# Performance work log

Hardware: AMD Instinct MI355X
Metric: run time of the kernel (lower is better)

## Reference

```python
import jax, jax.numpy as jnp
import numpy as np

B, T, C, H, L, V = 8, 512, 512, 8, 2, 512
DH = C // H
SCALE = 1.0 / np.sqrt(DH)


def _ln(x, g, b):
    mu = jnp.mean(x, -1, keepdims=True)
    var = jnp.mean((x - mu) ** 2, -1, keepdims=True)
    return (x - mu) * jax.lax.rsqrt(var + 1e-5) * g + b


def setup_inputs() -> dict:
    key = jax.random.key(0)
    ks = jax.random.split(key, 16)
    f = lambda k, shape: jax.random.normal(k, shape, jnp.float32) * 0.02
    return {
        "idx": jax.random.randint(ks[0], (B, T), 0, 4),
        "tok_emb": f(ks[1], (4, C)),
        "pos_emb": f(ks[2], (T, C)),
        "ln1_g": jnp.ones((L, C)), "ln1_b": jnp.zeros((L, C)),
        "Wq": f(ks[3], (L, C, C)), "bq": jnp.zeros((L, C)),
        "Wk": f(ks[4], (L, C, C)), "bk": jnp.zeros((L, C)),
        "Wv": f(ks[5], (L, C, C)), "bv": jnp.zeros((L, C)),
        "Wp": f(ks[6], (L, C, C)), "bp": jnp.zeros((L, C)),
        "ln2_g": jnp.ones((L, C)), "ln2_b": jnp.zeros((L, C)),
        "W1": f(ks[7], (L, C, 4 * C)), "b1": jnp.zeros((L, 4 * C)),
        "W2": f(ks[8], (L, 4 * C, C)), "b2": jnp.zeros((L, C)),
        "lnf_g": jnp.ones((C,)), "lnf_b": jnp.zeros((C,)),
        "Whead": f(ks[9], (C, V)),
        "steps": 4,
    }


def _block(x, p):
    (l1g, l1b, wq, bq, wk, bk, wv, bv, wp, bp,
     l2g, l2b, w1, b1, w2, b2) = p
    # attention (mask buffer is all ones in the original -> full attention)
    xn = _ln(x, l1g, l1b)
    q = (xn @ wq + bq).reshape(B, T, H, DH)
    k = (xn @ wk + bk).reshape(B, T, H, DH)
    v = (xn @ wv + bv).reshape(B, T, H, DH)
    att = jnp.einsum('bqhd,bkhd->bhqk', q, k) * SCALE
    att = jax.nn.softmax(att, axis=-1)
    y = jnp.einsum('bhqk,bkhd->bqhd', att, v).reshape(B, T, C)
    x = x + y @ wp + bp
    # MLP with exact (erf) GELU, matching torch nn.GELU default
    h = jax.nn.gelu(_ln(x, l2g, l2b) @ w1 + b1, approximate=False)
    return x + h @ w2 + b2


def reference(idx, tok_emb, pos_emb, ln1_g, ln1_b, Wq, bq, Wk, bk, Wv, bv,
              Wp, bp, ln2_g, ln2_b, W1, b1, W2, b2, lnf_g, lnf_b, Whead,
              steps):
    params = (ln1_g, ln1_b, Wq, bq, Wk, bk, Wv, bv, Wp, bp,
              ln2_g, ln2_b, W1, b1, W2, b2)
    x = tok_emb[idx] + pos_emb[None, :, :]

    def run_blocks(x):
        def step(x, p):
            return _block(x, p), None
        x, _ = jax.lax.scan(step, x, params)
        return x

    for _ in range(steps):  # recurrent application of the whole stack
        x = run_blocks(x)
    x = _ln(x, lnf_g, lnf_b)
    return x @ Whead  # logits [B, T, V]
```

## Files before the change

kernel.cpp:

```cpp
#include <hip/hip_runtime.h>
#include <hip/hip_bf16.h>
#include <math.h>

#define BB 8
#define TT 512
#define CC 512
#define HH 8
#define DH 64
#define LL 2
#define VV 512
#define NSTEPS 4
#define BT (BB*TT)
#define FF (4*CC)

typedef unsigned short u16;
typedef __bf16 bf16x8 __attribute__((ext_vector_type(8)));
typedef float f32x4 __attribute__((ext_vector_type(4)));

static __device__ __forceinline__ u16 f2bf(float f) {
    unsigned int u = __float_as_uint(f);
    unsigned int r = (u + 0x7fffu + ((u >> 16) & 1u)) >> 16;
    return (u16)r;
}

static __device__ __forceinline__ void async16(const void* g, void* l) {
    __builtin_amdgcn_global_load_lds((__attribute__((address_space(1))) void*)g,
                                     (__attribute__((address_space(3))) void*)l, 16, 0, 0);
}

static __device__ __forceinline__ int swzp(int r) { return (r ^ (r >> 2)) & 7; }

__global__ void embed_kernel(const int* __restrict__ idx, const float* __restrict__ tok,
                             const float* __restrict__ pos, float* __restrict__ x) {
    int bt = blockIdx.x;
    int t  = threadIdx.x;
    int token = idx[bt];
    int posrow = bt % TT;
    x[(size_t)bt*CC + t]       = tok[token*CC + t]       + pos[posrow*CC + t];
    x[(size_t)bt*CC + t + 256] = tok[token*CC + t + 256] + pos[posrow*CC + t + 256];
}

__global__ void ln_kernel(const float* __restrict__ x, const float* __restrict__ g,
                          const float* __restrict__ b, u16* __restrict__ out) {
    int row = blockIdx.x;
    int t = threadIdx.x;
    const float* xr = x + (size_t)row * CC;
    float v0 = xr[t], v1 = xr[t + 256];
    __shared__ float rs[256], rq[256];
    rs[t] = v0 + v1;
    rq[t] = v0 * v0 + v1 * v1;
    __syncthreads();
    for (int off = 128; off > 0; off >>= 1) {
        if (t < off) { rs[t] += rs[t + off]; rq[t] += rq[t + off]; }
        __syncthreads();
    }
    float mean = rs[0] * (1.0f / CC);
    float var  = rq[0] * (1.0f / CC) - mean * mean;
    float inv  = rsqrtf(var + 1e-5f);
    out[(size_t)row*CC + t]       = f2bf((v0 - mean) * inv * g[t]       + b[t]);
    out[(size_t)row*CC + t + 256] = f2bf((v1 - mean) * inv * g[t + 256] + b[t + 256]);
}

__global__ __launch_bounds__(256)
void cast_all_kernel(const float* __restrict__ Wq, const float* __restrict__ Wk,
                     const float* __restrict__ Wv, const float* __restrict__ Wp,
                     const float* __restrict__ W1, const float* __restrict__ W2,
                     const float* __restrict__ Wh,
                     u16* w_qkvt, u16* w_pt, u16* w_1t, u16* w_2t, u16* w_ht) {
    int bid = blockIdx.x;
    const float* src; u16* dst; int K, N, i0, j0;
    const size_t wcc = (size_t)CC*CC, wcf = (size_t)CC*FF;
    if (bid < 1536) {
        int l = bid / 768, r = bid % 768;
        if (r < 256) {
            int m = r / 64, t = r % 64;
            K = CC; N = CC;
            i0 = (t / 8) * 64; j0 = (t % 8) * 64;
            if      (m == 0) { src = Wq + l*wcc; dst = w_qkvt + (size_t)l*3*wcc; }
            else if (m == 1) { src = Wk + l*wcc; dst = w_qkvt + (size_t)l*3*wcc + wcc; }
            else if (m == 2) { src = Wv + l*wcc; dst = w_qkvt + (size_t)l*3*wcc + 2*wcc; }
            else             { src = Wp + l*wcc; dst = w_pt + (size_t)l*wcc; }
        } else if (r < 512) {
            int t = r - 256;
            K = CC; N = FF;
            i0 = (t / 32) * 64; j0 = (t % 32) * 64;
            src = W1 + l*wcf; dst = w_1t + (size_t)l*wcf;
        } else {
            int t = r - 512;
            K = FF; N = CC;
            i0 = (t / 8) * 64; j0 = (t % 8) * 64;
            src = W2 + l*wcf; dst = w_2t + (size_t)l*wcf;
        }
    } else {
        int t = bid - 1536;
        K = CC; N = CC;
        i0 = (t / 8) * 64; j0 = (t % 8) * 64;
        src = Wh; dst = w_ht;
    }
    __shared__ float tile[64][65];
    int tt = threadIdx.x;
    int rr = tt >> 2, cg = (tt & 3) * 16;
#pragma unroll
    for (int i = 0; i < 16; i++)
        tile[rr][cg + i] = src[(size_t)(i0 + rr) * N + j0 + cg + i];
    __syncthreads();
#pragma unroll
    for (int i = 0; i < 16; i++)
        dst[(size_t)(j0 + rr) * K + i0 + cg + i] = f2bf(tile[cg + i][rr]);
}

template<int BM, int BN, int THREADS, int WROWS, int WCOLS, int EPI>
__global__ __launch_bounds__(THREADS, 6)
void gemm_bt_kernel(const u16* __restrict__ A, const u16* __restrict__ Bt,
                    int N, int K,
                    const float* __restrict__ bias, const float* __restrict__ biask,
                    const float* __restrict__ biasv,
                    float* outf, u16* outq, u16* outk, u16* outvt) {
    constexpr int WTM = BM / WROWS, WTN = BN / WCOLS;
    constexpr int TM = WTM / 16, TN = WTN / 16;
    static_assert(THREADS / 4 == 2 * BM, "A staged in exactly one call");
    static_assert(THREADS == WROWS * WCOLS * 64, "wave grid");
    __shared__ u16 lds_a[2][2][BM][32];
    __shared__ u16 lds_b[2][2][BN][32];
    int tid = threadIdx.x;
    int wid = tid >> 6, lane = tid & 63;
    int quad = lane >> 4, l15 = lane & 15;
    int wm = (wid % WROWS) * WTM, wn = (wid / WROWS) * WTN;

    int NBN = N / BN;
    int lin = blockIdx.x;
    int x8 = lin & 7, slot = lin >> 3;
    int bn = slot % NBN;
    int bm = (slot / NBN) * 8 + x8;

    const int fr = tid >> 2;
    const int c2 = tid & 3;
    const size_t a0 = (size_t)bm * BM, b0 = (size_t)bn * BN;

    auto stage = [&](int buf, int kt) {
        {
            int ks2 = fr / BM, row = fr % BM;
            int g = (ks2 * 4 + c2) ^ swzp(row);
            async16(&A[(a0 + row) * K + kt + g * 8], &lds_a[buf][ks2][row][c2 * 8]);
        }
#pragma unroll
        for (int i = 0; i < (2 * BN) / (THREADS / 4); i++) {
            int f = fr + i * (THREADS / 4);
            int ks2 = f / BN, row = f % BN;
            int g = (ks2 * 4 + c2) ^ swzp(row);
            async16(&Bt[(b0 + row) * K + kt + g * 8], &lds_b[buf][ks2][row][c2 * 8]);
        }
    };

    f32x4 zero = {0.f, 0.f, 0.f, 0.f};
    f32x4 acc[TM][TN];
#pragma unroll
    for (int mi = 0; mi < TM; mi++)
#pragma unroll
        for (int ni = 0; ni < TN; ni++) acc[mi][ni] = zero;

    stage(0, 0);
    __syncthreads();
    const int NKT = K / 64;
    for (int kt = 0; kt < NKT; kt++) {
        int cur = kt & 1;
        if (kt + 1 < NKT) stage(cur ^ 1, (kt + 1) * 64);
#pragma unroll
        for (int ks = 0; ks < 2; ks++) {
            bf16x8 af[TM], bfr[TN];
#pragma unroll
            for (int mi = 0; mi < TM; mi++) {
                int row = wm + mi*16 + l15;
                int lc = (ks*4 + quad) ^ swzp(row);
                af[mi] = *(const bf16x8*)&lds_a[cur][lc >> 2][row][(lc & 3) * 8];
            }
#pragma unroll
            for (int ni = 0; ni < TN; ni++) {
                int row = wn + ni*16 + l15;
                int lc = (ks*4 + quad) ^ swzp(row);
                bfr[ni] = *(const bf16x8*)&lds_b[cur][lc >> 2][row][(lc & 3) * 8];
            }
#pragma unroll
            for (int mi = 0; mi < TM; mi++)
#pragma unroll
                for (int ni = 0; ni < TN; ni++)
                    acc[mi][ni] = __builtin_amdgcn_mfma_f32_16x16x32_bf16(af[mi], bfr[ni], acc[mi][ni], 0, 0, 0);
        }
        __syncthreads();
    }

#pragma unroll
    for (int mi = 0; mi < TM; mi++)
#pragma unroll
        for (int ni = 0; ni < TN; ni++)
#pragma unroll
            for (int i = 0; i < 4; i++) {
                int row = bm*BM + wm + mi*16 + quad*4 + i;
                int col = bn*BN + wn + ni*16 + l15;
                float v = acc[mi][ni][i];
                if (EPI == 0) {
                    int region = col >> 9, cl = col & 511;
                    if (region == 0) {
                        v = (v + bias[cl]) * 0.125f;
                        outq[(size_t)row*512 + cl] = f2bf(v);
                    } else if (region == 1) {
                        v += biask[cl];
                        outk[(size_t)row*512 + cl] = f2bf(v);
                    } else {
                        v += biasv[cl];
                        int bb = row >> 9, tpos = row & 511, hh = cl >> 6, dh = cl & 63;
                        outvt[(((size_t)(bb*8 + hh)*64 + dh) << 9) + tpos] = f2bf(v);
                    }
                } else if (EPI == 1) {
                    size_t idx2 = (size_t)row * N + col;
                    v += bias[col] + outf[idx2];
                    outf[idx2] = v;
                } else if (EPI == 2) {
                    v += bias[col];
                    v = 0.5f * v * (1.0f + erff(v * 0.70710678118654752f));
                    outq[(size_t)row * N + col] = f2bf(v);
                } else {
                    outf[(size_t)row * N + col] = v;
                }
            }
}

__global__ __launch_bounds__(256)
void attn_mfma_kernel(const u16* __restrict__ q, const u16* __restrict__ k,
                      const u16* __restrict__ vt, u16* __restrict__ y) {
    __shared__ u16 lq[64][64];
    __shared__ u16 lk[2][64][64];
    __shared__ u16 lv[2][64][64];
    __shared__ u16 lp[4][16][72];
    int qt = blockIdx.x, h = blockIdx.y, b = blockIdx.z;
    int tid = threadIdx.x;
    int wid = tid >> 6, lane = tid & 63;
    int quad = lane >> 4, l15 = lane & 15;
    const int sr = tid >> 3;
    const int sc = (tid & 7) * 8;
    const int gsc = (((tid & 7) ^ swzp(sr)) << 3);

    auto stageKV = [&](int buf, int kt) {
#pragma unroll
        for (int c = 0; c < 2; c++) {
            async16(&k[(size_t)(b*TT + kt*64 + c*32 + sr)*CC + h*DH + gsc], &lk[buf][c*32 + sr][sc]);
            async16(&vt[((size_t)((b*HH + h)*DH + c*32 + sr))*TT + kt*64 + gsc], &lv[buf][c*32 + sr][sc]);
        }
    };

#pragma unroll
    for (int c = 0; c < 2; c++)
        async16(&q[(size_t)(b*TT + qt*64 + c*32 + sr)*CC + h*DH + gsc], &lq[c*32 + sr][sc]);
    stageKV(0, 0);
    __syncthreads();

    f32x4 zero = {0.f, 0.f, 0.f, 0.f};
    f32x4 acc_o[4];
    float m_st[4], l_st[4];
#pragma unroll
    for (int i = 0; i < 4; i++) { m_st[i] = -INFINITY; l_st[i] = 0.f; }
#pragma unroll
    for (int ni = 0; ni < 4; ni++) acc_o[ni] = zero;

    const int rowq = wid*16 + l15;
    const int pq = swzp(rowq);

    for (int kt = 0; kt < TT/64; kt++) {
        int cur = kt & 1;
        if (kt + 1 < TT/64) stageKV(cur ^ 1, kt + 1);

        f32x4 s[4];
#pragma unroll
        for (int ni = 0; ni < 4; ni++) s[ni] = zero;
#pragma unroll
        for (int ks = 0; ks < 2; ks++) {
            int lcq = (ks*4 + quad) ^ pq;
            bf16x8 aq = *(const bf16x8*)&lq[rowq][lcq * 8];
            bf16x8 bfr[4];
#pragma unroll
            for (int ni = 0; ni < 4; ni++) {
                int rowk = ni*16 + l15;
                int lck = (ks*4 + quad) ^ swzp(rowk);
                bfr[ni] = *(const bf16x8*)&lk[cur][rowk][lck * 8];
            }
#pragma unroll
            for (int ni = 0; ni < 4; ni++)
                s[ni] = __builtin_amdgcn_mfma_f32_16x16x32_bf16(aq, bfr[ni], s[ni], 0, 0, 0);
        }

#pragma unroll
        for (int i = 0; i < 4; i++) {
            float mx = -INFINITY;
#pragma unroll
            for (int ni = 0; ni < 4; ni++) mx = fmaxf(mx, s[ni][i]);
#pragma unroll
            for (int off = 1; off < 16; off <<= 1) mx = fmaxf(mx, __shfl_xor(mx, off));
            float mn = fmaxf(m_st[i], mx);
            float al = __expf(m_st[i] - mn);
            float rs = 0.f;
#pragma unroll
            for (int ni = 0; ni < 4; ni++) {
                float p = __expf(s[ni][i] - mn);
                s[ni][i] = p;
                rs += p;
            }
#pragma unroll
            for (int off = 1; off < 16; off <<= 1) rs += __shfl_xor(rs, off);
            l_st[i] = l_st[i] * al + rs;
            m_st[i] = mn;
#pragma unroll
            for (int ni = 0; ni < 4; ni++) acc_o[ni][i] *= al;
        }

#pragma unroll
        for (int ni = 0; ni < 4; ni++)
#pragma unroll
            for (int i = 0; i < 4; i++)
                lp[wid][quad*4 + i][ni*16 + l15] = f2bf(s[ni][i]);

#pragma unroll
        for (int ks = 0; ks < 2; ks++) {
            bf16x8 pa = *(const bf16x8*)&lp[wid][l15][ks*32 + quad*8];
            bf16x8 vb[4];
#pragma unroll
            for (int ni = 0; ni < 4; ni++) {
                int rowv = ni*16 + l15;
                int lcv = (ks*4 + quad) ^ swzp(rowv);
                vb[ni] = *(const bf16x8*)&lv[cur][rowv][lcv * 8];
            }
#pragma unroll
            for (int ni = 0; ni < 4; ni++)
                acc_o[ni] = __builtin_amdgcn_mfma_f32_16x16x32_bf16(pa, vb[ni], acc_o[ni], 0, 0, 0);
        }
        __syncthreads();
    }

#pragma unroll
    for (int i = 0; i < 4; i++) {
        float inv = 1.0f / l_st[i];
#pragma unroll
        for (int ni = 0; ni < 4; ni++) {
            int qrow = qt*64 + wid*16 + quad*4 + i;
            int col  = h*DH + ni*16 + l15;
            y[(size_t)(b*TT + qrow)*CC + col] = f2bf(acc_o[ni][i] * inv);
        }
    }
}

extern "C" void kernel_launch(void* const* d_in, const int* in_sizes, int n_in,
                              void* d_out, int out_size, void* d_ws, size_t ws_size,
                              hipStream_t stream) {
    const int*   idx   = (const int*)d_in[0];
    const float* tok   = (const float*)d_in[1];
    const float* pos   = (const float*)d_in[2];
    const float* ln1g  = (const float*)d_in[3];
    const float* ln1b  = (const float*)d_in[4];
    const float* Wq    = (const float*)d_in[5];
    const float* bq    = (const float*)d_in[6];
    const float* Wk    = (const float*)d_in[7];
    const float* bk    = (const float*)d_in[8];
    const float* Wv    = (const float*)d_in[9];
    const float* bv    = (const float*)d_in[10];
    const float* Wp    = (const float*)d_in[11];
    const float* bp    = (const float*)d_in[12];
    const float* ln2g  = (const float*)d_in[13];
    const float* ln2b  = (const float*)d_in[14];
    const float* W1    = (const float*)d_in[15];
    const float* b1    = (const float*)d_in[16];
    const float* W2    = (const float*)d_in[17];
    const float* b2    = (const float*)d_in[18];
    const float* lnfg  = (const float*)d_in[19];
    const float* lnfb  = (const float*)d_in[20];
    const float* Whead = (const float*)d_in[21];

    float* x  = (float*)d_ws;
    u16* xn   = (u16*)(x + (size_t)BT*CC);
    u16* R    = xn + (size_t)BT*CC;
    u16* qb   = R;
    u16* kb   = R + (size_t)BT*CC;
    u16* vtb  = R + (size_t)2*BT*CC;
    u16* hb   = R;
    u16* w_qkvt = R + (size_t)4*BT*CC;
    u16* w_pt   = w_qkvt + (size_t)2*3*CC*CC;
    u16* w_1t   = w_pt   + (size_t)2*CC*CC;
    u16* w_2t   = w_1t   + (size_t)2*CC*FF;
    u16* w_ht   = w_2t   + (size_t)2*FF*CC;

    cast_all_kernel<<<1600, 256, 0, stream>>>(Wq, Wk, Wv, Wp, W1, W2, Whead,
                                              w_qkvt, w_pt, w_1t, w_2t, w_ht);
    embed_kernel<<<BT, 256, 0, stream>>>(idx, tok, pos, x);

    const int g_qkv  = (3*CC/128) * (BT/64);
    const int g_fc1  = (FF/128)   * (BT/64);
    const int g_proj = (CC/64)    * (BT/32);
    const int g_fc2  = (CC/64)    * (BT/32);
    const int g_head = (VV/64)    * (BT/32);

    for (int s = 0; s < NSTEPS; s++) {
        for (int l = 0; l < LL; l++) {
            ln_kernel<<<BT, 256, 0, stream>>>(x, ln1g + l*CC, ln1b + l*CC, xn);
            gemm_bt_kernel<64,128,512,2,4,0><<<g_qkv, 512, 0, stream>>>(
                xn, w_qkvt + (size_t)l*3*CC*CC, 3*CC, CC,
                bq + l*CC, bk + l*CC, bv + l*CC, nullptr, qb, kb, vtb);
            attn_mfma_kernel<<<dim3(TT/64, HH, BB), 256, 0, stream>>>(qb, kb, vtb, xn);
            gemm_bt_kernel<32,64,256,2,2,1><<<g_proj, 256, 0, stream>>>(
                xn, w_pt + (size_t)l*CC*CC, CC, CC,
                bp + l*CC, nullptr, nullptr, x, nullptr, nullptr, nullptr);
            ln_kernel<<<BT, 256, 0, stream>>>(x, ln2g + l*CC, ln2b + l*CC, xn);
            gemm_bt_kernel<64,128,512,2,4,2><<<g_fc1, 512, 0, stream>>>(
                xn, w_1t + (size_t)l*CC*FF, FF, CC,
                b1 + (size_t)l*FF, nullptr, nullptr, nullptr, hb, nullptr, nullptr);
            gemm_bt_kernel<32,64,256,2,2,1><<<g_fc2, 256, 0, stream>>>(
                hb, w_2t + (size_t)l*FF*CC, CC, FF,
                b2 + l*CC, nullptr, nullptr, x, nullptr, nullptr, nullptr);
        }
    }

    ln_kernel<<<BT, 256, 0, stream>>>(x, lnfg, lnfb, xn);
    gemm_bt_kernel<32,64,256,2,2,3><<<g_head, 256, 0, stream>>>(
        xn, w_ht, VV, CC, nullptr, nullptr, nullptr, (float*)d_out, nullptr, nullptr, nullptr);
}
```

Before: 950.0 us.

## Fuse LayerNorm into GEMM A-operand loading and shrink QKV/FC1 tiles

Removes the standalone LayerNorm kernels. Each GEMM that consumes a normalized input now computes per-row mean and inverse std itself, stages fp32 rows of x into LDS, and normalizes and converts to bf16 while building the MFMA A fragments. This drops a kernel launch and a round trip through the bf16 xn buffer per LayerNorm. The cost is higher LDS footprint, because A is held in fp32 and gamma/beta are also kept in LDS, plus redundant statistics work in every column block. The QKV and FC1 GEMMs move from 64x128 tiles with 512 threads to 32x128 tiles with 256 threads, which doubles the grid and changes occupancy hints.

New measurement: 1.167 ms. 1.23x slower.

```diff
diff --git a/kernel.cpp b/kernel.cpp
--- a/kernel.cpp
+++ b/kernel.cpp
@@ -16,6 +16,7 @@
 typedef unsigned short u16;
 typedef __bf16 bf16x8 __attribute__((ext_vector_type(8)));
 typedef float f32x4 __attribute__((ext_vector_type(4)));
+typedef u16 u16x8 __attribute__((ext_vector_type(8)));
 
 static __device__ __forceinline__ u16 f2bf(float f) {
     unsigned int u = __float_as_uint(f);
@@ -38,27 +39,6 @@
     int posrow = bt % TT;
     x[(size_t)bt*CC + t]       = tok[token*CC + t]       + pos[posrow*CC + t];
     x[(size_t)bt*CC + t + 256] = tok[token*CC + t + 256] + pos[posrow*CC + t + 256];
-}
-
-__global__ void ln_kernel(const float* __restrict__ x, const float* __restrict__ g,
-                          const float* __restrict__ b, u16* __restrict__ out) {
-    int row = blockIdx.x;
-    int t = threadIdx.x;
-    const float* xr = x + (size_t)row * CC;
-    float v0 = xr[t], v1 = xr[t + 256];
-    __shared__ float rs[256], rq[256];
-    rs[t] = v0 + v1;
-    rq[t] = v0 * v0 + v1 * v1;
-    __syncthreads();
-    for (int off = 128; off > 0; off >>= 1) {
-        if (t < off) { rs[t] += rs[t + off]; rq[t] += rq[t + off]; }
-        __syncthreads();
-    }
-    float mean = rs[0] * (1.0f / CC);
-    float var  = rq[0] * (1.0f / CC) - mean * mean;
-    float inv  = rsqrtf(var + 1e-5f);
-    out[(size_t)row*CC + t]       = f2bf((v0 - mean) * inv * g[t]       + b[t]);
-    out[(size_t)row*CC + t + 256] = f2bf((v1 - mean) * inv * g[t + 256] + b[t + 256]);
 }
 
 __global__ __launch_bounds__(256)
@@ -109,19 +89,24 @@
         dst[(size_t)(j0 + rr) * K + i0 + cg + i] = f2bf(tile[cg + i][rr]);
 }
 
-template<int BM, int BN, int THREADS, int WROWS, int WCOLS, int EPI>
-__global__ __launch_bounds__(THREADS, 6)
-void gemm_bt_kernel(const u16* __restrict__ A, const u16* __restrict__ Bt,
-                    int N, int K,
+template<int BM, int BN, int THREADS, int WROWS, int WCOLS, int EPI, bool LNA, int MINW>
+__global__ __launch_bounds__(THREADS, MINW)
+void gemm_bt_kernel(const u16* __restrict__ A, const float* __restrict__ xsrc,
+                    const float* __restrict__ gamma, const float* __restrict__ beta,
+                    const u16* __restrict__ Bt, int N, int K,
                     const float* __restrict__ bias, const float* __restrict__ biask,
                     const float* __restrict__ biasv,
                     float* outf, u16* outq, u16* outk, u16* outvt) {
     constexpr int WTM = BM / WROWS, WTN = BN / WCOLS;
     constexpr int TM = WTM / 16, TN = WTN / 16;
-    static_assert(THREADS / 4 == 2 * BM, "A staged in exactly one call");
     static_assert(THREADS == WROWS * WCOLS * 64, "wave grid");
-    __shared__ u16 lds_a[2][2][BM][32];
-    __shared__ u16 lds_b[2][2][BN][32];
+    static_assert(!LNA || (BM == 32 && THREADS == 256 && TM == 1), "LNA shape");
+    static_assert(LNA || THREADS / 4 == 2 * BM, "A staged in exactly one call");
+    __shared__ u16   lds_a [LNA ? 1 : 2*2*BM*32];
+    __shared__ float lds_af[LNA ? 2*2*32*32 : 1];
+    __shared__ u16   lds_b [2*2*BN*32];
+    __shared__ float lgam[LNA ? 512 : 1], lbet[LNA ? 512 : 1];
+    __shared__ float sstat[2][BM];
     int tid = threadIdx.x;
     int wid = tid >> 6, lane = tid & 63;
     int quad = lane >> 4, l15 = lane & 15;
@@ -133,22 +118,34 @@
     int bn = slot % NBN;
     int bm = (slot / NBN) * 8 + x8;
 
-    const int fr = tid >> 2;
-    const int c2 = tid & 3;
     const size_t a0 = (size_t)bm * BM, b0 = (size_t)bn * BN;
+    float myMean = 0.f, myInv = 0.f;
 
     auto stage = [&](int buf, int kt) {
-        {
+        if constexpr (LNA) {
+            int row = tid >> 3, ch = tid & 7;
+            int p = swzp(row);
+#pragma unroll
+            for (int ks2 = 0; ks2 < 2; ks2++)
+                async16(&xsrc[(a0 + row) * CC + kt + ks2*32 + ((ch ^ p) << 2)],
+                        &lds_af[(((buf*2 + ks2)*32 + row) << 5) + ch*4]);
+        } else {
+            int fr = tid >> 2, c2 = tid & 3;
             int ks2 = fr / BM, row = fr % BM;
             int g = (ks2 * 4 + c2) ^ swzp(row);
-            async16(&A[(a0 + row) * K + kt + g * 8], &lds_a[buf][ks2][row][c2 * 8]);
-        }
-#pragma unroll
-        for (int i = 0; i < (2 * BN) / (THREADS / 4); i++) {
-            int f = fr + i * (THREADS / 4);
-            int ks2 = f / BN, row = f % BN;
-            int g = (ks2 * 4 + c2) ^ swzp(row);
-            async16(&Bt[(b0 + row) * K + kt + g * 8], &lds_b[buf][ks2][row][c2 * 8]);
+            async16(&A[(a0 + row) * K + kt + g * 8],
+                    &lds_a[(((buf*2 + ks2)*BM + row) << 5) + c2*8]);
+        }
+        {
+            int fr = tid >> 2, c2 = tid & 3;
+#pragma unroll
+            for (int i = 0; i < (2 * BN) / (THREADS / 4); i++) {
+                int f = fr + i * (THREADS / 4);
+                int ks2 = f / BN, row = f % BN;
+                int g = (ks2 * 4 + c2) ^ swzp(row);
+                async16(&Bt[(b0 + row) * K + kt + g * 8],
+                        &lds_b[(((buf*2 + ks2)*BN + row) << 5) + c2*8]);
+            }
         }
     };
 
@@ -158,6 +155,37 @@
     for (int mi = 0; mi < TM; mi++)
 #pragma unroll
         for (int ni = 0; ni < TN; ni++) acc[mi][ni] = zero;
+
+    if constexpr (LNA) {
+        if (tid < 128) {
+            ((f32x4*)lgam)[tid] = ((const f32x4*)gamma)[tid];
+            ((f32x4*)lbet)[tid] = ((const f32x4*)beta)[tid];
+        }
+        int hw = tid >> 5, l32 = tid & 31;
+#pragma unroll
+        for (int rr = 0; rr < 4; rr++) {
+            int row = hw * 4 + rr;
+            const float* xr = xsrc + (a0 + row) * CC;
+            float s = 0.f, sq = 0.f;
+#pragma unroll
+            for (int i = 0; i < 4; i++) {
+                f32x4 v = ((const f32x4*)xr)[l32*4 + i];
+#pragma unroll
+                for (int j = 0; j < 4; j++) { s += v[j]; sq += v[j]*v[j]; }
+            }
+#pragma unroll
+            for (int off = 1; off < 32; off <<= 1) { s += __shfl_xor(s, off); sq += __shfl_xor(sq, off); }
+            if (l32 == 0) {
+                float mean = s * (1.0f / CC);
+                float var  = sq * (1.0f / CC) - mean * mean;
+                sstat[0][row] = mean;
+                sstat[1][row] = rsqrtf(var + 1e-5f);
+            }
+        }
+        __syncthreads();
+        myMean = sstat[0][wm + l15];
+        myInv  = sstat[1][wm + l15];
+    }
 
     stage(0, 0);
     __syncthreads();
@@ -168,17 +196,38 @@
 #pragma unroll
         for (int ks = 0; ks < 2; ks++) {
             bf16x8 af[TM], bfr[TN];
-#pragma unroll
-            for (int mi = 0; mi < TM; mi++) {
-                int row = wm + mi*16 + l15;
-                int lc = (ks*4 + quad) ^ swzp(row);
-                af[mi] = *(const bf16x8*)&lds_a[cur][lc >> 2][row][(lc & 3) * 8];
+            if constexpr (LNA) {
+                int row = wm + l15;
+                int p = swzp(row);
+                const float* base = &lds_af[((cur*2 + ks)*32 + row) << 5];
+                f32x4 av0 = *(const f32x4*)&base[(((quad<<1)    ) ^ p) << 2];
+                f32x4 av1 = *(const f32x4*)&base[(((quad<<1) | 1) ^ p) << 2];
+                int kofs = kt*64 + ks*32 + quad*8;
+                f32x4 g0 = *(const f32x4*)&lgam[kofs];
+                f32x4 g1 = *(const f32x4*)&lgam[kofs + 4];
+                f32x4 e0 = *(const f32x4*)&lbet[kofs];
+                f32x4 e1 = *(const f32x4*)&lbet[kofs + 4];
+                union { u16x8 u; bf16x8 b; } cvt;
+#pragma unroll
+                for (int j = 0; j < 4; j++)
+                    cvt.u[j] = f2bf((av0[j] - myMean) * myInv * g0[j] + e0[j]);
+#pragma unroll
+                for (int j = 0; j < 4; j++)
+                    cvt.u[4 + j] = f2bf((av1[j] - myMean) * myInv * g1[j] + e1[j]);
+                af[0] = cvt.b;
+            } else {
+#pragma unroll
+                for (int mi = 0; mi < TM; mi++) {
+                    int row = wm + mi*16 + l15;
+                    int lc = (ks*4 + quad) ^ swzp(row);
+                    af[mi] = *(const bf16x8*)&lds_a[(((cur*2 + (lc >> 2))*BM + row) << 5) + (lc & 3)*8];
+                }
             }
 #pragma unroll
             for (int ni = 0; ni < TN; ni++) {
                 int row = wn + ni*16 + l15;
                 int lc = (ks*4 + quad) ^ swzp(row);
-                bfr[ni] = *(const bf16x8*)&lds_b[cur][lc >> 2][row][(lc & 3) * 8];
+                bfr[ni] = *(const bf16x8*)&lds_b[(((cur*2 + (lc >> 2))*BN + row) << 5) + (lc & 3)*8];
             }
 #pragma unroll
             for (int mi = 0; mi < TM; mi++)
@@ -390,33 +439,35 @@
                                               w_qkvt, w_pt, w_1t, w_2t, w_ht);
     embed_kernel<<<BT, 256, 0, stream>>>(idx, tok, pos, x);
 
-    const int g_qkv  = (3*CC/128) * (BT/64);
-    const int g_fc1  = (FF/128)   * (BT/64);
+    const int g_qkv  = (3*CC/128) * (BT/32);
+    const int g_fc1  = (FF/128)   * (BT/32);
     const int g_proj = (CC/64)    * (BT/32);
     const int g_fc2  = (CC/64)    * (BT/32);
     const int g_head = (VV/64)    * (BT/32);
 
     for (int s = 0; s < NSTEPS; s++) {
         for (int l = 0; l < LL; l++) {
-            ln_kernel<<<BT, 256, 0, stream>>>(x, ln1g + l*CC, ln1b + l*CC, xn);
-            gemm_bt_kernel<64,128,512,2,4,0><<<g_qkv, 512, 0, stream>>>(
-                xn, w_qkvt + (size_t)l*3*CC*CC, 3*CC, CC,
+            gemm_bt_kernel<32,128,256,2,2,0,true,3><<<g_qkv, 256, 0, stream>>>(
+                nullptr, x, ln1g + l*CC, ln1b + l*CC,
+                w_qkvt + (size_t)l*3*CC*CC, 3*CC, CC,
                 bq + l*CC, bk + l*CC, bv + l*CC, nullptr, qb, kb, vtb);
             attn_mfma_kernel<<<dim3(TT/64, HH, BB), 256, 0, stream>>>(qb, kb, vtb, xn);
-            gemm_bt_kernel<32,64,256,2,2,1><<<g_proj, 256, 0, stream>>>(
-                xn, w_pt + (size_t)l*CC*CC, CC, CC,
+            gemm_bt_kernel<32,64,256,2,2,1,false,6><<<g_proj, 256, 0, stream>>>(
+                xn, nullptr, nullptr, nullptr,
+                w_pt + (size_t)l*CC*CC, CC, CC,
                 bp + l*CC, nullptr, nullptr, x, nullptr, nullptr, nullptr);
-            ln_kernel<<<BT, 256, 0, stream>>>(x, ln2g + l*CC, ln2b + l*CC, xn);
-            gemm_bt_kernel<64,128,512,2,4,2><<<g_fc1, 512, 0, stream>>>(
-                xn, w_1t + (size_t)l*CC*FF, FF, CC,
+            gemm_bt_kernel<32,128,256,2,2,2,true,3><<<g_fc1, 256, 0, stream>>>(
+                nullptr, x, ln2g + l*CC, ln2b + l*CC,
+                w_1t + (size_t)l*CC*FF, FF, CC,
                 b1 + (size_t)l*FF, nullptr, nullptr, nullptr, hb, nullptr, nullptr);
-            gemm_bt_kernel<32,64,256,2,2,1><<<g_fc2, 256, 0, stream>>>(
-                hb, w_2t + (size_t)l*FF*CC, CC, FF,
+            gemm_bt_kernel<32,64,256,2,2,1,false,6><<<g_fc2, 256, 0, stream>>>(
+                hb, nullptr, nullptr, nullptr,
+                w_2t + (size_t)l*FF*CC, CC, FF,
                 b2 + l*CC, nullptr, nullptr, x, nullptr, nullptr, nullptr);
         }
     }
 
-    ln_kernel<<<BT, 256, 0, stream>>>(x, lnfg, lnfb, xn);
-    gemm_bt_kernel<32,64,256,2,2,3><<<g_head, 256, 0, stream>>>(
-        xn, w_ht, VV, CC, nullptr, nullptr, nullptr, (float*)d_out, nullptr, nullptr, nullptr);
-}
+    gemm_bt_kernel<32,64,256,2,2,3,true,4><<<g_head, 256, 0, stream>>>(
+        nullptr, x, lnfg, lnfb,
+        w_ht, VV, CC, nullptr, nullptr, nullptr, (float*)d_out, nullptr, nullptr, nullptr);
+}
```
